# Kernel optimization log

Hardware: AMD Instinct MI355X
Metric: run time of the kernel (lower is better)

Reference implementation:

```python
import jax, jax.numpy as jnp
import numpy as np

NEG_SLOPE = 0.2  # PyG GATConv default leaky_relu slope
EPS = 1e-16


def gat_conv(x, W, att_src, att_dst, bias, src, dst, heads, out_ch, concat):
    """PyG-style GATConv (eval mode, self-loops already added).
    x: [N, F_in], W: [F_in, heads*out_ch], att_src/att_dst: [heads, out_ch], bias matches output.
    src/dst: [E] int edge endpoints (messages flow src -> dst).
    """
    N = x.shape[0]
    h = (x @ W).reshape(N, heads, out_ch)                 # [N, H, C]
    a_src = jnp.einsum('nhc,hc->nh', h, att_src)           # [N, H]
    a_dst = jnp.einsum('nhc,hc->nh', h, att_dst)           # [N, H]
    e = jax.nn.leaky_relu(a_src[src] + a_dst[dst], NEG_SLOPE)  # [E, H]
    # scatter-softmax over edges grouped by destination node
    emax = jax.ops.segment_max(e, dst, num_segments=N)     # [N, H]
    e = jnp.exp(e - emax[dst])
    denom = jax.ops.segment_sum(e, dst, num_segments=N)    # [N, H]
    alpha = e / (denom[dst] + EPS)                         # [E, H]
    msg = alpha[:, :, None] * h[src]                       # [E, H, C]
    out = jax.ops.segment_sum(msg, dst, num_segments=N)    # [N, H, C]
    out = out.reshape(N, heads * out_ch) if concat else out.mean(axis=1)
    return out + bias


def _add_self_loops(edge_index, N):
    loop = jnp.arange(N, dtype=edge_index.dtype)
    src = jnp.concatenate([edge_index[0], loop])
    dst = jnp.concatenate([edge_index[1], loop])
    return src, dst


def setup_inputs() -> dict:
    key = jax.random.key(0)
    ks = jax.random.split(key, 12)
    N, F_in, E = 100000, 256, 3200000
    H1, C1 = 2, 16
    C2 = 40  # num_classes
    x = jax.random.normal(ks[0], (N, F_in), dtype=jnp.float32)
    edge_index = jax.random.randint(ks[1], (2, E), 0, N, dtype=jnp.int32)
    s1 = 1.0 / np.sqrt(F_in)
    s2 = 1.0 / np.sqrt(H1 * C1)
    W1 = jax.random.normal(ks[2], (F_in, H1 * C1), dtype=jnp.float32) * s1
    att_src1 = jax.random.normal(ks[3], (H1, C1), dtype=jnp.float32) * s2
    att_dst1 = jax.random.normal(ks[4], (H1, C1), dtype=jnp.float32) * s2
    b1 = jnp.zeros((H1 * C1,), dtype=jnp.float32)
    W2 = jax.random.normal(ks[5], (H1 * C1, C2), dtype=jnp.float32) * s2
    att_src2 = jax.random.normal(ks[6], (1, C2), dtype=jnp.float32) * 0.15
    att_dst2 = jax.random.normal(ks[7], (1, C2), dtype=jnp.float32) * 0.15
    b2 = jnp.zeros((C2,), dtype=jnp.float32)
    return {"x": x, "edge_index": edge_index, "W1": W1, "att_src1": att_src1,
            "att_dst1": att_dst1, "b1": b1, "W2": W2, "att_src2": att_src2,
            "att_dst2": att_dst2, "b2": b2}


def reference(x, edge_index, W1, att_src1, att_dst1, b1, W2, att_src2, att_dst2, b2):
    N = x.shape[0]
    src, dst = _add_self_loops(edge_index, N)
    h = gat_conv(x, W1, att_src1, att_dst1, b1, src, dst, heads=2, out_ch=16, concat=True)
    h = jax.nn.relu(h)
    # F.dropout / attention dropout are identity in eval mode
    out = gat_conv(h, W2, att_src2, att_dst2, b2, src, dst, heads=1, out_ch=40, concat=False)
    return jax.nn.log_softmax(out, axis=1)
```

## Files before the change

kernel.cpp:

```cpp
#include <hip/hip_runtime.h>
#include <math.h>

#define FIN 256
#define F1  32
#define H1  2
#define C1  16
#define C2  40
#define MAXDEG 96
#define NEG_SLOPE 0.2f
#define GAT_EPS 1e-16f
#define G1_NODES 32

__device__ __forceinline__ float lrelu(float v) { return v >= 0.f ? v : NEG_SLOPE * v; }

__global__ void k_fill_adj(const int* __restrict__ ei, int E, int N,
                           int* __restrict__ deg, int* __restrict__ adj) {
    int j = blockIdx.x * blockDim.x + threadIdx.x;
    int total = E + N;
    if (j >= total) return;
    int s, d;
    if (j < E) { s = ei[j]; d = ei[E + j]; }
    else       { s = j - E; d = s; }
    int pos = atomicAdd(&deg[d], 1);
    if (pos < MAXDEG) adj[d * MAXDEG + pos] = s;
}

__global__ __launch_bounds__(256) void k_gemm1(const float* __restrict__ x,
                                               const float* __restrict__ W1,
                                               float* __restrict__ h1, int N) {
    __shared__ float xs[G1_NODES * FIN];
    __shared__ float Ws[FIN * F1];
    int tid = threadIdx.x;
    int node0 = blockIdx.x * G1_NODES;

    const float4* W4 = (const float4*)W1;
    float4* Ws4 = (float4*)Ws;
    for (int i = tid; i < FIN * F1 / 4; i += 256) Ws4[i] = W4[i];

    const float4* x4 = (const float4*)x;
    float4* xs4 = (float4*)xs;
    for (int i = tid; i < G1_NODES * FIN / 4; i += 256) {
        int r = i >> 6;
        int n = node0 + r;
        float4 v = make_float4(0.f, 0.f, 0.f, 0.f);
        if (n < N) v = x4[(size_t)n * 64 + (i & 63)];
        xs4[i] = v;
    }
    __syncthreads();

    int ln = tid >> 3;
    int c0 = (tid & 7) * 4;
    float a0 = 0.f, a1 = 0.f, a2 = 0.f, a3 = 0.f;
    for (int k = 0; k < FIN; k += 4) {
        float4 xv = *(const float4*)&xs[ln * FIN + k];
        float4 w0 = *(const float4*)&Ws[(k + 0) * F1 + c0];
        float4 w1 = *(const float4*)&Ws[(k + 1) * F1 + c0];
        float4 w2 = *(const float4*)&Ws[(k + 2) * F1 + c0];
        float4 w3 = *(const float4*)&Ws[(k + 3) * F1 + c0];
        a0 += xv.x * w0.x + xv.y * w1.x + xv.z * w2.x + xv.w * w3.x;
        a1 += xv.x * w0.y + xv.y * w1.y + xv.z * w2.y + xv.w * w3.y;
        a2 += xv.x * w0.z + xv.y * w1.z + xv.z * w2.z + xv.w * w3.z;
        a3 += xv.x * w0.w + xv.y * w1.w + xv.z * w2.w + xv.w * w3.w;
    }
    int n = node0 + ln;
    if (n < N) {
        float4 o = make_float4(a0, a1, a2, a3);
        *(float4*)&h1[(size_t)n * F1 + c0] = o;
    }
}

__global__ void k_attdots1(const float* __restrict__ h1,
                           const float* __restrict__ attS, const float* __restrict__ attD,
                           float* __restrict__ aS, float* __restrict__ aD, int N) {
    int idx = blockIdx.x * blockDim.x + threadIdx.x;
    if (idx >= N * H1) return;
    int n = idx >> 1, h = idx & 1;
    const float* hp = h1 + (size_t)n * F1 + h * C1;
    const float* sp = attS + h * C1;
    const float* dp = attD + h * C1;
    float s = 0.f, d = 0.f;
#pragma unroll
    for (int c = 0; c < C1; c++) { float v = hp[c]; s += v * sp[c]; d += v * dp[c]; }
    aS[idx] = s; aD[idx] = d;
}

__global__ __launch_bounds__(256) void k_agg1(const float* __restrict__ h1,
                                              const int* __restrict__ adj,
                                              const int* __restrict__ deg,
                                              const float* __restrict__ aS,
                                              const float* __restrict__ aD,
                                              const float* __restrict__ b1,
                                              float* __restrict__ h1r, int N) {
    int warp = threadIdx.x >> 6;
    int lane = threadIdx.x & 63;
    int node = blockIdx.x * 4 + warp;
    if (node >= N) return;
    int dg = min(deg[node], MAXDEG);
    float2 adp = *(const float2*)&aD[node * 2];
    const int* ap = adj + (size_t)node * MAXDEG;

    int s0 = 0, s1 = 0;
    float e00 = -INFINITY, e01 = -INFINITY, e10 = -INFINITY, e11 = -INFINITY;
    if (lane < dg) {
        s0 = ap[lane];
        float2 as = *(const float2*)&aS[2 * s0];
        e00 = lrelu(as.x + adp.x); e01 = lrelu(as.y + adp.y);
    }
    if (lane + 64 < dg) {
        s1 = ap[lane + 64];
        float2 as = *(const float2*)&aS[2 * s1];
        e10 = lrelu(as.x + adp.x); e11 = lrelu(as.y + adp.y);
    }
    float m0 = fmaxf(e00, e10), m1 = fmaxf(e01, e11);
#pragma unroll
    for (int off = 32; off; off >>= 1) {
        m0 = fmaxf(m0, __shfl_xor(m0, off));
        m1 = fmaxf(m1, __shfl_xor(m1, off));
    }
    float w00 = (lane < dg)      ? __expf(e00 - m0) : 0.f;
    float w01 = (lane < dg)      ? __expf(e01 - m1) : 0.f;
    float w10 = (lane + 64 < dg) ? __expf(e10 - m0) : 0.f;
    float w11 = (lane + 64 < dg) ? __expf(e11 - m1) : 0.f;
    float sw0 = w00 + w10, sw1 = w01 + w11;
#pragma unroll
    for (int off = 32; off; off >>= 1) {
        sw0 += __shfl_xor(sw0, off);
        sw1 += __shfl_xor(sw1, off);
    }

    int eg = lane >> 3;
    int cg = lane & 7;
    int head = cg >> 2;
    float4 acc = make_float4(0.f, 0.f, 0.f, 0.f);
    for (int j0 = 0; j0 < dg; j0 += 8) {
        int j = j0 + eg;
        int sl = j & 63;
        int s; float w;
        if (j0 < 64) {
            s = __shfl(s0, sl);
            float wA = __shfl(w00, sl);
            float wB = __shfl(w01, sl);
            w = head ? wB : wA;
        } else {
            s = __shfl(s1, sl);
            float wA = __shfl(w10, sl);
            float wB = __shfl(w11, sl);
            w = head ? wB : wA;
        }
        float4 hv = *(const float4*)&h1[(size_t)s * F1 + cg * 4];
        acc.x += w * hv.x; acc.y += w * hv.y; acc.z += w * hv.z; acc.w += w * hv.w;
    }
#pragma unroll
    for (int off = 8; off < 64; off <<= 1) {
        acc.x += __shfl_xor(acc.x, off);
        acc.y += __shfl_xor(acc.y, off);
        acc.z += __shfl_xor(acc.z, off);
        acc.w += __shfl_xor(acc.w, off);
    }
    if (eg == 0) {
        float swh = head ? sw1 : sw0;
        float inv = 1.f / (swh + GAT_EPS);
        float4 bv = *(const float4*)&b1[cg * 4];
        float4 o;
        o.x = fmaxf(acc.x * inv + bv.x, 0.f);
        o.y = fmaxf(acc.y * inv + bv.y, 0.f);
        o.z = fmaxf(acc.z * inv + bv.z, 0.f);
        o.w = fmaxf(acc.w * inv + bv.w, 0.f);
        *(float4*)&h1r[(size_t)node * F1 + cg * 4] = o;
    }
}

__global__ __launch_bounds__(320) void k_gemm2(const float* __restrict__ h1r,
                                               const float* __restrict__ W2,
                                               float* __restrict__ h2, int N) {
    __shared__ float hs[8 * F1];
    __shared__ float Ws[F1 * C2];
    int tid = threadIdx.x;
    int node0 = blockIdx.x * 8;
    for (int i = tid; i < F1 * C2; i += 320) Ws[i] = W2[i];
    if (tid < 8 * F1) {
        int r = tid >> 5;
        int n = node0 + r;
        hs[tid] = (n < N) ? h1r[(size_t)n * F1 + (tid & 31)] : 0.f;
    }
    __syncthreads();
    int node = tid / C2;
    int col  = tid - node * C2;
    int n = node0 + node;
    if (n < N) {
        float acc = 0.f;
#pragma unroll
        for (int k = 0; k < F1; k++) acc += hs[node * F1 + k] * Ws[k * C2 + col];
        h2[(size_t)n * C2 + col] = acc;
    }
}

__global__ void k_attdots2(const float* __restrict__ h2,
                           const float* __restrict__ attS, const float* __restrict__ attD,
                           float* __restrict__ aS, float* __restrict__ aD, int N) {
    int n = blockIdx.x * blockDim.x + threadIdx.x;
    if (n >= N) return;
    const float* hp = h2 + (size_t)n * C2;
    float s = 0.f, d = 0.f;
#pragma unroll
    for (int c = 0; c < C2; c++) { float v = hp[c]; s += v * attS[c]; d += v * attD[c]; }
    aS[n] = s; aD[n] = d;
}

__global__ __launch_bounds__(256) void k_agg2(const float* __restrict__ h2,
                                              const int* __restrict__ adj,
                                              const int* __restrict__ deg,
                                              const float* __restrict__ aS,
                                              const float* __restrict__ aD,
                                              const float* __restrict__ b2,
                                              float* __restrict__ out, int N) {
    int warp = threadIdx.x >> 6;
    int lane = threadIdx.x & 63;
    int node = blockIdx.x * 4 + warp;
    if (node >= N) return;
    int dg = min(deg[node], MAXDEG);
    float ad = aD[node];
    const int* ap = adj + (size_t)node * MAXDEG;

    int s0 = 0, s1 = 0;
    float e0 = -INFINITY, e1 = -INFINITY;
    if (lane < dg)      { s0 = ap[lane];      e0 = lrelu(aS[s0] + ad); }
    if (lane + 64 < dg) { s1 = ap[lane + 64]; e1 = lrelu(aS[s1] + ad); }
    float m = fmaxf(e0, e1);
#pragma unroll
    for (int off = 32; off; off >>= 1) m = fmaxf(m, __shfl_xor(m, off));
    float w0 = (lane < dg)      ? __expf(e0 - m) : 0.f;
    float w1 = (lane + 64 < dg) ? __expf(e1 - m) : 0.f;
    float sw = w0 + w1;
#pragma unroll
    for (int off = 32; off; off >>= 1) sw += __shfl_xor(sw, off);

    int eg = lane >> 3;
    int cg = lane & 7;
    float4 acc = make_float4(0.f, 0.f, 0.f, 0.f);
    float acc4 = 0.f;
    for (int j0 = 0; j0 < dg; j0 += 8) {
        int j = j0 + eg;
        int sl = j & 63;
        int s; float w;
        if (j0 < 64) { s = __shfl(s0, sl); w = __shfl(w0, sl); }
        else         { s = __shfl(s1, sl); w = __shfl(w1, sl); }
        const float* hp = &h2[(size_t)s * C2];
        float4 hv = *(const float4*)&hp[cg * 4];
        float  h5 = hp[32 + cg];
        acc.x += w * hv.x; acc.y += w * hv.y; acc.z += w * hv.z; acc.w += w * hv.w;
        acc4  += w * h5;
    }
#pragma unroll
    for (int off = 8; off < 64; off <<= 1) {
        acc.x += __shfl_xor(acc.x, off);
        acc.y += __shfl_xor(acc.y, off);
        acc.z += __shfl_xor(acc.z, off);
        acc.w += __shfl_xor(acc.w, off);
        acc4  += __shfl_xor(acc4, off);
    }
    float inv = 1.f / (sw + GAT_EPS);
    float4 bv = *(const float4*)&b2[cg * 4];
    float  b5 = b2[32 + cg];
    float v0 = acc.x * inv + bv.x;
    float v1 = acc.y * inv + bv.y;
    float v2 = acc.z * inv + bv.z;
    float v3 = acc.w * inv + bv.w;
    float v4 = acc4  * inv + b5;

    float lm = fmaxf(fmaxf(fmaxf(v0, v1), fmaxf(v2, v3)), v4);
#pragma unroll
    for (int off = 1; off < 8; off <<= 1) lm = fmaxf(lm, __shfl_xor(lm, off));
    float ex = __expf(v0 - lm) + __expf(v1 - lm) + __expf(v2 - lm) +
               __expf(v3 - lm) + __expf(v4 - lm);
#pragma unroll
    for (int off = 1; off < 8; off <<= 1) ex += __shfl_xor(ex, off);
    float lse = lm + __logf(ex);
    if (eg == 0) {
        float* op = out + (size_t)node * C2;
        float4 o = make_float4(v0 - lse, v1 - lse, v2 - lse, v3 - lse);
        *(float4*)&op[cg * 4] = o;
        op[32 + cg] = v4 - lse;
    }
}

extern "C" void kernel_launch(void* const* d_in, const int* in_sizes, int n_in,
                              void* d_out, int out_size, void* d_ws, size_t ws_size,
                              hipStream_t stream) {
    const float* x    = (const float*)d_in[0];
    const int*   ei   = (const int*)d_in[1];
    const float* W1   = (const float*)d_in[2];
    const float* aS1w = (const float*)d_in[3];
    const float* aD1w = (const float*)d_in[4];
    const float* b1   = (const float*)d_in[5];
    const float* W2   = (const float*)d_in[6];
    const float* aS2w = (const float*)d_in[7];
    const float* aD2w = (const float*)d_in[8];
    const float* b2   = (const float*)d_in[9];
    const int N = in_sizes[0] / FIN;
    const int E = in_sizes[1] / 2;

    char* ws = (char*)d_ws;
    size_t off = 0;
    auto alloc = [&](size_t bytes) -> void* {
        void* p = ws + off;
        off = (off + bytes + 511) & ~(size_t)511;
        return p;
    };
    int*   deg = (int*)alloc(sizeof(int) * (size_t)N);
    int*   adj = (int*)alloc(sizeof(int) * (size_t)N * MAXDEG);
    float* h1  = (float*)alloc(sizeof(float) * (size_t)N * F1);
    float* aS1 = (float*)alloc(sizeof(float) * (size_t)N * H1);
    float* aD1 = (float*)alloc(sizeof(float) * (size_t)N * H1);
    float* h1r = (float*)alloc(sizeof(float) * (size_t)N * F1);
    float* h2  = (float*)alloc(sizeof(float) * (size_t)N * C2);
    float* aS2 = (float*)alloc(sizeof(float) * (size_t)N);
    float* aD2 = (float*)alloc(sizeof(float) * (size_t)N);

    hipMemsetAsync(deg, 0, sizeof(int) * (size_t)N, stream);
    int total = E + N;
    k_fill_adj<<<(total + 255) / 256, 256, 0, stream>>>(ei, E, N, deg, adj);
    k_gemm1<<<(N + G1_NODES - 1) / G1_NODES, 256, 0, stream>>>(x, W1, h1, N);
    k_attdots1<<<(N * H1 + 255) / 256, 256, 0, stream>>>(h1, aS1w, aD1w, aS1, aD1, N);
    k_agg1<<<(N + 3) / 4, 256, 0, stream>>>(h1, adj, deg, aS1, aD1, b1, h1r, N);
    k_gemm2<<<(N + 7) / 8, 320, 0, stream>>>(h1r, W2, h2, N);
    k_attdots2<<<(N + 255) / 256, 256, 0, stream>>>(h2, aS2w, aD2w, aS2, aD2, N);
    k_agg2<<<(N + 3) / 4, 256, 0, stream>>>(h2, adj, deg, aS2, aD2, b2, (float*)d_out, N);
}
```

Baseline: 595.3 us.

## Partition adjacency fill by destination range and fuse attention dots into GEMM1

```diff
diff --git a/kernel.cpp b/kernel.cpp
--- a/kernel.cpp
+++ b/kernel.cpp
@@ -10,24 +10,41 @@
 #define NEG_SLOPE 0.2f
 #define GAT_EPS 1e-16f
 #define G1_NODES 32
+#define FILL_BLOCKS 2048
 
 __device__ __forceinline__ float lrelu(float v) { return v >= 0.f ? v : NEG_SLOPE * v; }
 
-__global__ void k_fill_adj(const int* __restrict__ ei, int E, int N,
-                           int* __restrict__ deg, int* __restrict__ adj) {
-    int j = blockIdx.x * blockDim.x + threadIdx.x;
+__global__ __launch_bounds__(256) void k_fill_adj(const int* __restrict__ ei, int E, int N,
+                                                  int* __restrict__ deg, int* __restrict__ adj) {
+    int res = blockIdx.x & 7;
+    int nper = (N + 7) >> 3;
+    int lo = res * nper;
+    int hi = min(N, lo + nper);
     int total = E + N;
-    if (j >= total) return;
-    int s, d;
-    if (j < E) { s = ei[j]; d = ei[E + j]; }
-    else       { s = j - E; d = s; }
-    int pos = atomicAdd(&deg[d], 1);
-    if (pos < MAXDEG) adj[d * MAXDEG + pos] = s;
+    int stride = (gridDim.x >> 3) * blockDim.x;
+    for (int j = (blockIdx.x >> 3) * blockDim.x + threadIdx.x; j < total; j += stride) {
+        int d, s;
+        if (j < E) {
+            d = __builtin_nontemporal_load(&ei[E + j]);
+            s = 0;
+            if (d >= lo && d < hi) s = __builtin_nontemporal_load(&ei[j]);
+        } else {
+            d = j - E; s = d;
+        }
+        if (d >= lo && d < hi) {
+            int pos = atomicAdd(&deg[d], 1);
+            if (pos < MAXDEG) adj[d * MAXDEG + pos] = s;
+        }
+    }
 }
 
 __global__ __launch_bounds__(256) void k_gemm1(const float* __restrict__ x,
                                                const float* __restrict__ W1,
-                                               float* __restrict__ h1, int N) {
+                                               const float* __restrict__ attS,
+                                               const float* __restrict__ attD,
+                                               float* __restrict__ h1,
+                                               float* __restrict__ aS,
+                                               float* __restrict__ aD, int N) {
     __shared__ float xs[G1_NODES * FIN];
     __shared__ float Ws[FIN * F1];
     int tid = threadIdx.x;
@@ -62,26 +79,24 @@
         a2 += xv.x * w0.z + xv.y * w1.z + xv.z * w2.z + xv.w * w3.z;
         a3 += xv.x * w0.w + xv.y * w1.w + xv.z * w2.w + xv.w * w3.w;
     }
+
+    float4 sv = *(const float4*)&attS[c0];
+    float4 dv = *(const float4*)&attD[c0];
+    float ps = a0 * sv.x + a1 * sv.y + a2 * sv.z + a3 * sv.w;
+    float pd = a0 * dv.x + a1 * dv.y + a2 * dv.z + a3 * dv.w;
+    ps += __shfl_xor(ps, 1); ps += __shfl_xor(ps, 2);
+    pd += __shfl_xor(pd, 1); pd += __shfl_xor(pd, 2);
+    float po = __shfl_xor(ps, 4);
+    float qo = __shfl_xor(pd, 4);
+
     int n = node0 + ln;
     if (n < N) {
-        float4 o = make_float4(a0, a1, a2, a3);
-        *(float4*)&h1[(size_t)n * F1 + c0] = o;
-    }
-}
-
-__global__ void k_attdots1(const float* __restrict__ h1,
-                           const float* __restrict__ attS, const float* __restrict__ attD,
-                           float* __restrict__ aS, float* __restrict__ aD, int N) {
-    int idx = blockIdx.x * blockDim.x + threadIdx.x;
-    if (idx >= N * H1) return;
-    int n = idx >> 1, h = idx & 1;
-    const float* hp = h1 + (size_t)n * F1 + h * C1;
-    const float* sp = attS + h * C1;
-    const float* dp = attD + h * C1;
-    float s = 0.f, d = 0.f;
-#pragma unroll
-    for (int c = 0; c < C1; c++) { float v = hp[c]; s += v * sp[c]; d += v * dp[c]; }
-    aS[idx] = s; aD[idx] = d;
+        *(float4*)&h1[(size_t)n * F1 + c0] = make_float4(a0, a1, a2, a3);
+        if ((tid & 7) == 0) {
+            *(float2*)&aS[2 * (size_t)n] = make_float2(ps, po);
+            *(float2*)&aD[2 * (size_t)n] = make_float2(pd, qo);
+        }
+    }
 }
 
 __global__ __launch_bounds__(256) void k_agg1(const float* __restrict__ h1,
@@ -318,10 +333,8 @@
     float* aD2 = (float*)alloc(sizeof(float) * (size_t)N);
 
     hipMemsetAsync(deg, 0, sizeof(int) * (size_t)N, stream);
-    int total = E + N;
-    k_fill_adj<<<(total + 255) / 256, 256, 0, stream>>>(ei, E, N, deg, adj);
-    k_gemm1<<<(N + G1_NODES - 1) / G1_NODES, 256, 0, stream>>>(x, W1, h1, N);
-    k_attdots1<<<(N * H1 + 255) / 256, 256, 0, stream>>>(h1, aS1w, aD1w, aS1, aD1, N);
+    k_fill_adj<<<FILL_BLOCKS, 256, 0, stream>>>(ei, E, N, deg, adj);
+    k_gemm1<<<(N + G1_NODES - 1) / G1_NODES, 256, 0, stream>>>(x, W1, aS1w, aD1w, h1, aS1, aD1, N);
     k_agg1<<<(N + 3) / 4, 256, 0, stream>>>(h1, adj, deg, aS1, aD1, b1, h1r, N);
     k_gemm2<<<(N + 7) / 8, 320, 0, stream>>>(h1r, W2, h2, N);
     k_attdots2<<<(N + 255) / 256, 256, 0, stream>>>(h2, aS2w, aD2w, aS2, aD2, N);
```

Result: faster. 574.5 us (-3.5%).
